# Kernel tuning notes

Hardware: AMD Instinct MI355X
Metric: run time of the kernel (lower is better)

The kernel has to match this reference:

```python
import jax, jax.numpy as jnp
import numpy as np

ALPHA = 0.95
BETA = 0.9

def setup_inputs() -> dict:
    key = jax.random.key(0)
    k1, k2 = jax.random.split(key)
    B, T, I, O = 64, 1000, 512, 256
    inputs = jax.random.normal(k1, (B, T, I), dtype=jnp.float32)
    W = jax.random.normal(k2, (O, I), dtype=jnp.float32) * (1.0 / np.sqrt(I))
    return {"inputs": inputs, "W": W, "nb_steps": T}

def reference(inputs, W, nb_steps):
    B = inputs.shape[0]
    O = W.shape[0]
    # linear projection: h[b,t,o]
    h = jnp.einsum('bti,oi->bto', inputs, W)
    h_t = jnp.swapaxes(h, 0, 1)  # (T, B, O) for scan over time

    def step(carry, ht):
        flt, out = carry
        new_flt = ALPHA * flt + ht
        new_out = BETA * out + flt  # uses OLD flt, matching the torch loop
        return (new_flt, new_out), new_out

    init = (jnp.zeros((B, O), jnp.float32), jnp.zeros((B, O), jnp.float32))
    _, out_rec = jax.lax.scan(step, init, h_t)
    return jnp.swapaxes(out_rec, 0, 1)  # (B, T, O)
```

## Files before the change

kernel.cpp:

```cpp
#include <hip/hip_runtime.h>
#include <hip/hip_bf16.h>
#include <stdint.h>


#define ALPHA 0.95f
#define BETA  0.9f

constexpr int Bdim = 64, T = 1000, Idim = 512, Odim = 256;
constexpr int M = Bdim * T;
constexpr int C = 40, L = 25;

typedef short bf16x8 __attribute__((ext_vector_type(8)));
typedef float f32x4  __attribute__((ext_vector_type(4)));

__device__ inline uint32_t pk_bf16(float a, float b) {
  union { float f; uint32_t u; } x, y; x.f = a; y.f = b;
  uint32_t lo = (x.u + 0x7FFFu + ((x.u >> 16) & 1u)) >> 16;
  uint32_t hi = (y.u + 0x7FFFu + ((y.u >> 16) & 1u)) & 0xFFFF0000u;
  return lo | hi;
}
__device__ inline uint16_t f2bf(float a) {
  union { float f; uint32_t u; } x; x.f = a;
  return (uint16_t)((x.u + 0x7FFFu + ((x.u >> 16) & 1u)) >> 16);
}
__device__ inline float bf2f(uint16_t h) {
  union { uint32_t u; float f; } x; x.u = ((uint32_t)h) << 16;
  return x.f;
}

__device__ inline bf16x8 cvt8(float4 x0, float4 x1) {
  union { __hip_bfloat162 h[4]; bf16x8 v; } r;
  r.h[0] = __float22bfloat162_rn(make_float2(x0.x, x0.y));
  r.h[1] = __float22bfloat162_rn(make_float2(x0.z, x0.w));
  r.h[2] = __float22bfloat162_rn(make_float2(x1.x, x1.y));
  r.h[3] = __float22bfloat162_rn(make_float2(x1.z, x1.w));
  return r.v;
}

__global__ __launch_bounds__(256) void wconv(const float* __restrict__ W,
                                             uint16_t* __restrict__ Wbf) {
  int i = (blockIdx.x * 256 + threadIdx.x) * 8;
  float4 a = *(const float4*)(W + i);
  float4 b = *(const float4*)(W + i + 4);
  *(uint4*)(Wbf + i) = make_uint4(pk_bf16(a.x, a.y), pk_bf16(a.z, a.w),
                                  pk_bf16(b.x, b.y), pk_bf16(b.z, b.w));
}

__global__ __launch_bounds__(256, 3) void gemm_h(const float* __restrict__ A,
                                                 const uint16_t* __restrict__ Wbf,
                                                 uint16_t* __restrict__ H) {
  const int tid  = threadIdx.x;
  const int lane = tid & 63;
  const int w    = tid >> 6;
  const int l15  = lane & 15;
  const int quad = lane >> 4;
  const int rm   = blockIdx.x * 64;

  const float*    ap[4];
  const uint16_t* bp[4];
#pragma unroll
  for (int t = 0; t < 4; ++t) {
    ap[t] = A   + (size_t)(rm + t * 16 + l15) * Idim + quad * 8;
    bp[t] = Wbf + (size_t)(w * 64 + t * 16 + l15) * Idim + quad * 8;
  }

  f32x4 acc[4][4] = {};

  float4 ca[4][2];
#pragma unroll
  for (int t = 0; t < 4; ++t) {
    ca[t][0] = *(const float4*)(ap[t]);
    ca[t][1] = *(const float4*)(ap[t] + 4);
  }

#pragma unroll
  for (int ks = 0; ks < 16; ++ks) {
    bf16x8 bfr[4];
#pragma unroll
    for (int t = 0; t < 4; ++t) {
      union { uint4 u; bf16x8 v; } bb;
      bb.u = *(const uint4*)(bp[t] + ks * 32);
      bfr[t] = bb.v;
    }
    float4 na[4][2];
    if (ks < 15) {
      const int ko = (ks + 1) * 32;
#pragma unroll
      for (int t = 0; t < 4; ++t) {
        na[t][0] = *(const float4*)(ap[t] + ko);
        na[t][1] = *(const float4*)(ap[t] + ko + 4);
      }
    }
    bf16x8 af[4];
#pragma unroll
    for (int t = 0; t < 4; ++t) af[t] = cvt8(ca[t][0], ca[t][1]);
#pragma unroll
    for (int mt = 0; mt < 4; ++mt)
#pragma unroll
      for (int nt = 0; nt < 4; ++nt)
        acc[mt][nt] = __builtin_amdgcn_mfma_f32_16x16x32_bf16(af[mt], bfr[nt], acc[mt][nt], 0, 0, 0);
    if (ks < 15) {
#pragma unroll
      for (int t = 0; t < 4; ++t) { ca[t][0] = na[t][0]; ca[t][1] = na[t][1]; }
    }
  }

#pragma unroll
  for (int mt = 0; mt < 4; ++mt)
#pragma unroll
    for (int nt = 0; nt < 4; ++nt)
#pragma unroll
      for (int r = 0; r < 4; ++r) {
        int gm = rm + mt * 16 + quad * 4 + r;
        int gn = w * 64 + nt * 16 + l15;
        H[(size_t)gm * Odim + gn] = f2bf(acc[mt][nt][r]);
      }
}

constexpr double dpow(double x, int n) { double r = 1.0; for (int i = 0; i < n; ++i) r *= x; return r; }

__global__ __launch_bounds__(640) void scan_all(const uint16_t* __restrict__ H,
                                                float* __restrict__ Out) {
  constexpr float AL = (float)dpow(0.95, L);
  constexpr float BL = (float)dpow(0.90, L);
  constexpr float WL = (float)((dpow(0.95, L) - dpow(0.90, L)) / (0.95 - 0.90));
  __shared__ float2 St[C][64];

  const int b   = blockIdx.x >> 2;
  const int og  = blockIdx.x & 3;
  const int tid = threadIdx.x;
  const int c   = tid >> 4;
  const int ol  = tid & 15;

  const size_t base = ((size_t)b * T + c * L) * Odim + og * 64 + ol * 4;
  const ushort4* hp = (const ushort4*)(H + base);

  ushort4 hv[L];
  {
    float f[4] = {}, u[4] = {};
#pragma unroll
    for (int j = 0; j < L; ++j) {
      hv[j] = hp[j * 64];
      float h0 = bf2f(hv[j].x), h1 = bf2f(hv[j].y), h2 = bf2f(hv[j].z), h3 = bf2f(hv[j].w);
      float n0 = BETA * u[0] + f[0]; f[0] = ALPHA * f[0] + h0; u[0] = n0;
      float n1 = BETA * u[1] + f[1]; f[1] = ALPHA * f[1] + h1; u[1] = n1;
      float n2 = BETA * u[2] + f[2]; f[2] = ALPHA * f[2] + h2; u[2] = n2;
      float n3 = BETA * u[3] + f[3]; f[3] = ALPHA * f[3] + h3; u[3] = n3;
    }
#pragma unroll
    for (int i = 0; i < 4; ++i) St[c][ol * 4 + i] = make_float2(f[i], u[i]);
  }
  __syncthreads();

  if (tid < 64) {
    float f = 0.f, u = 0.f;
#pragma unroll
    for (int cc = 0; cc < C; ++cc) {
      float2 s = St[cc][tid];
      St[cc][tid] = make_float2(f, u);
      float nu = BL * u + WL * f + s.y;
      f = AL * f + s.x;
      u = nu;
    }
  }
  __syncthreads();

  {
    float f[4], u[4];
#pragma unroll
    for (int i = 0; i < 4; ++i) { float2 s = St[c][ol * 4 + i]; f[i] = s.x; u[i] = s.y; }
    float4* op = (float4*)(Out + base);
#pragma unroll
    for (int j = 0; j < L; ++j) {
      float h0 = bf2f(hv[j].x), h1 = bf2f(hv[j].y), h2 = bf2f(hv[j].z), h3 = bf2f(hv[j].w);
      float4 o4;
      o4.x = BETA * u[0] + f[0]; f[0] = ALPHA * f[0] + h0; u[0] = o4.x;
      o4.y = BETA * u[1] + f[1]; f[1] = ALPHA * f[1] + h1; u[1] = o4.y;
      o4.z = BETA * u[2] + f[2]; f[2] = ALPHA * f[2] + h2; u[2] = o4.z;
      o4.w = BETA * u[3] + f[3]; f[3] = ALPHA * f[3] + h3; u[3] = o4.w;
      op[j * 64] = o4;
    }
  }
}

extern "C" void kernel_launch(void* const* d_in, const int* in_sizes, int n_in,
                              void* d_out, int out_size, void* d_ws, size_t ws_size,
                              hipStream_t stream) {
  const float* A = (const float*)d_in[0];
  const float* W = (const float*)d_in[1];
  float* Out = (float*)d_out;

  uint16_t* H   = (uint16_t*)d_ws;
  uint16_t* Wbf = H + (size_t)M * Odim;

  wconv<<<Odim * Idim / (256 * 8), 256, 0, stream>>>(W, Wbf);
  gemm_h<<<M / 64, 256, 0, stream>>>(A, Wbf, H);
  scan_all<<<Bdim * 4, 640, 0, stream>>>(H, Out);
}
```

Baseline: 273.2 us.

## Stage GEMM tiles in LDS via direct global-to-LDS loads with swizzle, 128-row tiles

The projection GEMM now stages A (fp32) and W (bf16) tiles in shared memory using global_load_lds 16-byte direct loads. An XOR swizzle on the LDS layout avoids bank conflicts. The row tile per block doubles from 64 to 128, so each wave computes an 8x4 grid of MFMA tiles and reuses each loaded W fragment across twice as many rows. The aim is less redundant global traffic for W and more MFMA work per load. In exchange there are two block barriers per K step with no double buffering, more accumulator registers, and a lower occupancy hint.

After: 226.1 us. 1.21x faster.

```diff
diff --git a/kernel.cpp b/kernel.cpp
--- a/kernel.cpp
+++ b/kernel.cpp
@@ -27,6 +27,10 @@
   union { uint32_t u; float f; } x; x.u = ((uint32_t)h) << 16;
   return x.f;
 }
+
+#define GLD16(g, l) __builtin_amdgcn_global_load_lds(                         \
+    (const __attribute__((address_space(1))) uint32_t*)(g),                   \
+    (__attribute__((address_space(3))) uint32_t*)(l), 16, 0, 0)
 
 __device__ inline bf16x8 cvt8(float4 x0, float4 x1) {
   union { __hip_bfloat162 h[4]; bf16x8 v; } r;
@@ -46,67 +50,72 @@
                                   pk_bf16(b.x, b.y), pk_bf16(b.z, b.w));
 }
 
-__global__ __launch_bounds__(256, 3) void gemm_h(const float* __restrict__ A,
+__global__ __launch_bounds__(256, 2) void gemm_h(const float* __restrict__ A,
                                                  const uint16_t* __restrict__ Wbf,
                                                  uint16_t* __restrict__ H) {
+  __shared__ float    As[128 * 32];
+  __shared__ uint16_t Bs[256 * 32];
+
   const int tid  = threadIdx.x;
   const int lane = tid & 63;
   const int w    = tid >> 6;
   const int l15  = lane & 15;
   const int quad = lane >> 4;
-  const int rm   = blockIdx.x * 64;
-
-  const float*    ap[4];
-  const uint16_t* bp[4];
-#pragma unroll
-  for (int t = 0; t < 4; ++t) {
-    ap[t] = A   + (size_t)(rm + t * 16 + l15) * Idim + quad * 8;
-    bp[t] = Wbf + (size_t)(w * 64 + t * 16 + l15) * Idim + quad * 8;
-  }
-
-  f32x4 acc[4][4] = {};
-
-  float4 ca[4][2];
-#pragma unroll
-  for (int t = 0; t < 4; ++t) {
-    ca[t][0] = *(const float4*)(ap[t]);
-    ca[t][1] = *(const float4*)(ap[t] + 4);
-  }
-
-#pragma unroll
-  for (int ks = 0; ks < 16; ++ks) {
+  const int rm   = blockIdx.x * 128;
+
+  const float* asrc[4];
+  char*        aldst[4];
+#pragma unroll
+  for (int i = 0; i < 4; ++i) {
+    int row = w * 32 + i * 8 + (lane >> 3);
+    int g   = (lane & 7) ^ (row & 7);
+    asrc[i]  = A + (size_t)(rm + row) * Idim + g * 4;
+    aldst[i] = (char*)As + w * 4096 + i * 1024;
+  }
+  const uint16_t* bsrc[4];
+  char*           bldst[4];
+#pragma unroll
+  for (int i = 0; i < 4; ++i) {
+    int row = w * 64 + i * 16 + (lane >> 2);
+    int g   = (lane & 3) ^ (row & 3);
+    bsrc[i]  = Wbf + (size_t)row * Idim + g * 8;
+    bldst[i] = (char*)Bs + w * 4096 + i * 1024;
+  }
+
+  f32x4 acc[8][4] = {};
+
+  for (int k0 = 0; k0 < Idim; k0 += 32) {
+    __syncthreads();
+#pragma unroll
+    for (int i = 0; i < 4; ++i) GLD16(asrc[i] + k0, aldst[i]);
+#pragma unroll
+    for (int i = 0; i < 4; ++i) GLD16(bsrc[i] + k0, bldst[i]);
+    __syncthreads();
+
     bf16x8 bfr[4];
 #pragma unroll
-    for (int t = 0; t < 4; ++t) {
-      union { uint4 u; bf16x8 v; } bb;
-      bb.u = *(const uint4*)(bp[t] + ks * 32);
-      bfr[t] = bb.v;
-    }
-    float4 na[4][2];
-    if (ks < 15) {
-      const int ko = (ks + 1) * 32;
-#pragma unroll
-      for (int t = 0; t < 4; ++t) {
-        na[t][0] = *(const float4*)(ap[t] + ko);
-        na[t][1] = *(const float4*)(ap[t] + ko + 4);
-      }
-    }
-    bf16x8 af[4];
-#pragma unroll
-    for (int t = 0; t < 4; ++t) af[t] = cvt8(ca[t][0], ca[t][1]);
-#pragma unroll
-    for (int mt = 0; mt < 4; ++mt)
+    for (int nt = 0; nt < 4; ++nt) {
+      int n = w * 64 + nt * 16 + l15;
+      bfr[nt] = *(const bf16x8*)&Bs[n * 32 + ((quad ^ (n & 3)) * 8)];
+    }
+    bf16x8 af[8];
+#pragma unroll
+    for (int mt = 0; mt < 8; ++mt) {
+      int m  = mt * 16 + l15;
+      int s0 = (2 * quad) ^ (m & 7);
+      float4 x0 = *(const float4*)&As[m * 32 + s0 * 4];
+      float4 x1 = *(const float4*)&As[m * 32 + (s0 ^ 1) * 4];
+      af[mt] = ((m & 1) == (m & 1)) ? cvt8(x0, x1) : cvt8(x0, x1);
+    }
+#pragma unroll
+    for (int mt = 0; mt < 8; ++mt)
 #pragma unroll
       for (int nt = 0; nt < 4; ++nt)
         acc[mt][nt] = __builtin_amdgcn_mfma_f32_16x16x32_bf16(af[mt], bfr[nt], acc[mt][nt], 0, 0, 0);
-    if (ks < 15) {
-#pragma unroll
-      for (int t = 0; t < 4; ++t) { ca[t][0] = na[t][0]; ca[t][1] = na[t][1]; }
-    }
-  }
-
-#pragma unroll
-  for (int mt = 0; mt < 4; ++mt)
+  }
+
+#pragma unroll
+  for (int mt = 0; mt < 8; ++mt)
 #pragma unroll
     for (int nt = 0; nt < 4; ++nt)
 #pragma unroll
@@ -194,6 +203,6 @@
   uint16_t* Wbf = H + (size_t)M * Odim;
 
   wconv<<<Odim * Idim / (256 * 8), 256, 0, stream>>>(W, Wbf);
-  gemm_h<<<M / 64, 256, 0, stream>>>(A, Wbf, H);
+  gemm_h<<<M / 128, 256, 0, stream>>>(A, Wbf, H);
   scan_all<<<Bdim * 4, 640, 0, stream>>>(H, Out);
 }
```
